# Kernel optimization log

Hardware: AMD Instinct MI355X
Metric: run time of the kernel (lower is better)

Reference implementation:

```python
import jax, jax.numpy as jnp
import numpy as np

H = 1024  # hidden_dims

def _gru_scan(xs, h0, wih, whh, bih, bhh):
    # xs: (T, D_in); torch GRU gate order: r, z, n
    xp = xs @ wih.T + bih  # (T, 3H), precomputed input projection
    def step(h, xp_t):
        hh = h @ whh.T + bhh
        r = jax.nn.sigmoid(xp_t[:H] + hh[:H])
        z = jax.nn.sigmoid(xp_t[H:2 * H] + hh[H:2 * H])
        n = jnp.tanh(xp_t[2 * H:] + r * hh[2 * H:])
        h_new = (1.0 - z) * n + z * h
        return h_new, None
    h_last, _ = jax.lax.scan(step, h0, xp)
    return h_last

def _lstm_step(h_in, wih, bih, bhh):
    # single-step nn.LSTM(H, H) with zero initial (h0, c0): Whh terms vanish, biases remain.
    # torch LSTM gate order: i, f, g, o
    xp = h_in @ wih.T + bih + bhh  # (4H,)
    i = jax.nn.sigmoid(xp[:H])
    g = jnp.tanh(xp[2 * H:3 * H])
    o = jax.nn.sigmoid(xp[3 * H:])
    c = i * g  # f * c0 == 0
    return o * jnp.tanh(c)

def setup_inputs() -> dict:
    key = jax.random.key(0)
    ks = jax.random.split(key, 20)
    T, D_w, D_i = 8192, 32, 32
    s = 0.05
    inp = {
        "weather_window": jax.random.normal(ks[0], (T, 1, D_w), jnp.float32),
        "infect_window": jax.random.normal(ks[1], (T, 1, D_i), jnp.float32),
        "time_window": jax.random.uniform(ks[2], (T, 1), jnp.float32),
        "h_init": jax.random.normal(ks[3], (1, 1, H), jnp.float32),
        "enc_w1": jax.random.normal(ks[4], (512, 64), jnp.float32) * s,
        "enc_b1": jax.random.normal(ks[5], (512,), jnp.float32) * s,
        "enc_w2": jax.random.normal(ks[6], (1024, 512), jnp.float32) * s,
        "enc_b2": jax.random.normal(ks[7], (1024,), jnp.float32) * s,
        "gru_wih": jax.random.normal(ks[8], (3 * H, H), jnp.float32) * s,
        "gru_whh": jax.random.normal(ks[9], (3 * H, H), jnp.float32) * s,
        "gru_bih": jax.random.normal(ks[10], (3 * H,), jnp.float32) * s,
        "gru_bhh": jax.random.normal(ks[11], (3 * H,), jnp.float32) * s,
        "lstm_wih": jax.random.normal(ks[12], (4 * H, H), jnp.float32) * s,
        "lstm_bih": jax.random.normal(ks[13], (4 * H,), jnp.float32) * s,
        "lstm_bhh": jax.random.normal(ks[14], (4 * H,), jnp.float32) * s,
        "dec_w1": jax.random.normal(ks[15], (512, 1024), jnp.float32) * s,
        "dec_b1": jax.random.normal(ks[16], (512,), jnp.float32) * s,
        "dec_w2": jax.random.normal(ks[17], (8, 512), jnp.float32) * s,
        "dec_b2": jax.random.normal(ks[18], (8,), jnp.float32) * s,
    }
    return inp

def reference(weather_window, infect_window, time_window, h_init,
              enc_w1, enc_b1, enc_w2, enc_b2,
              gru_wih, gru_whh, gru_bih, gru_bhh,
              lstm_wih, lstm_bih, lstm_bhh,
              dec_w1, dec_b1, dec_w2, dec_b2):
    T = weather_window.shape[0]
    # use_diff_time = False branch
    data_window = jnp.concatenate([weather_window, infect_window], axis=2)  # (T,1,64)
    rev = data_window[::-1]  # flip(0)
    # Encoder FC stack
    x = jax.nn.relu(rev @ enc_w1.T + enc_b1)
    x = jax.nn.relu(x @ enc_w2.T + enc_b2)  # (T,1,H)
    # Encoder GRU -> final hidden state
    h_enc = _gru_scan(x[:, 0, :], h_init[0, 0], gru_wih, gru_whh, gru_bih, gru_bhh)  # (H,)
    def step(h, _):
        h_new = _lstm_step(h, lstm_wih, lstm_bih, lstm_bhh)
        return h_new, h_new
    _, hs_tail = jax.lax.scan(step, h_enc, None, length=T - 1)  # (T-1, H)
    hs = jnp.concatenate([h_enc[None, :], hs_tail], axis=0)  # (T, H)
    hs = hs[:, None, None, :]  # (T,1,1,H), matches torch.stack of (1,1,H)
    # Decoder FC stack
    y = jax.nn.relu(hs @ dec_w1.T + dec_b1)
    y = y @ dec_w2.T + dec_b2  # (T,1,1,8)
    return y
```

## Files before the change

### kernel.cpp

```cpp
#include <hip/hip_runtime.h>
#include <hip/hip_bf16.h>
#include <math.h>

#define T_STEPS 8192
#define HDIM    1024
#define GW      128
#define NSLOT   512
#define SLOT_PITCH 256
#define NREP    8
#define REP_STRIDE ((size_t)2 * NSLOT * SLOT_PITCH)

#define OFF_REV   ((size_t)0)
#define OFF_X1    ((size_t)2097152)
#define OFF_B     ((size_t)18874368)
#define OFF_C     ((size_t)52428800)
#define WS_NEEDED ((size_t)153092096)

typedef float f4 __attribute__((ext_vector_type(4)));

__device__ inline float sigm(float x)   { return 1.0f / (1.0f + __expf(-x)); }
__device__ inline float tanh_f(float x) { float e = __expf(2.0f * x); return 1.0f - 2.0f / (e + 1.0f); }

__device__ inline f4* slot_ptr(char* base, int rep, int b, int k) {
    return (f4*)(base + (size_t)rep * REP_STRIDE + ((size_t)b * NSLOT + k) * SLOT_PITCH);
}

__device__ inline void store_cohr(f4* p, f4 v) {
    asm volatile("global_store_dwordx4 %0, %1, off sc0 sc1"
                 :: "v"(p), "v"(v) : "memory");
}

__device__ inline void poll_pair(const f4* p, unsigned want, f4& a, f4& b) {
    for (;;) {
        f4 va, vb;
        asm volatile("global_load_dwordx4 %0, %2, off sc0 sc1\n\t"
                     "global_load_dwordx4 %1, %2, off offset:256 sc0 sc1\n\t"
                     "s_waitcnt vmcnt(0)"
                     : "=&v"(va), "=&v"(vb) : "v"(p) : "memory");
        if (__float_as_uint(va.w) == want && __float_as_uint(vb.w) == want) {
            a = va; b = vb; return;
        }
        __builtin_amdgcn_s_sleep(1);
    }
}

__global__ void build_rev(const float* __restrict__ wea, const float* __restrict__ inf,
                          float* __restrict__ rev) {
    int idx = blockIdx.x * blockDim.x + threadIdx.x;
    if (idx >= T_STEPS * 64) return;
    int t = idx >> 6, c = idx & 63;
    int ts = T_STEPS - 1 - t;
    rev[idx] = (c < 32) ? wea[ts * 32 + c] : inf[ts * 32 + (c - 32)];
}

__global__ void seed_slots(const float* __restrict__ h0, char* __restrict__ sb) {
    int i = blockIdx.x * blockDim.x + threadIdx.x;
    int rep = i >> 10;
    int j   = i & 1023;
    if (rep < NREP) {
        if (j < NSLOT) {
            f4 v;
            v.x = h0[2 * j]; v.y = h0[2 * j + 1]; v.z = 0.0f;
            v.w = __uint_as_float(0u);
            store_cohr(slot_ptr(sb, rep, 0, j), v);
        } else {
            f4 v;
            v.x = 0.f; v.y = 0.f; v.z = 0.f;
            v.w = __uint_as_float(0xFFFFFFFFu);
            store_cohr(slot_ptr(sb, rep, 1, j - NSLOT), v);
        }
    }
}

__global__ __launch_bounds__(256) void gemm_bias_act(
    const float* __restrict__ A, const float* __restrict__ W,
    const float* __restrict__ bias, float* __restrict__ C,
    int M, int N, int K, int relu)
{
    __shared__ float As[32][68];
    __shared__ float Ws[32][68];
    const int tid = threadIdx.x;
    const int tx = tid & 15, ty = tid >> 4;
    const int bm = blockIdx.y, bn = blockIdx.x;
    const float* Ab = A + (size_t)bm * 64 * K;
    const float* Wb = W + (size_t)bn * 64 * K;
    float acc[4][4] = {};

    for (int k0 = 0; k0 < K; k0 += 32) {
#pragma unroll
        for (int q = 0; q < 2; ++q) {
            int idx = tid * 2 + q;
            int row = idx >> 3;
            int kc  = (idx & 7) << 2;
            float4 av = *(const float4*)(Ab + (size_t)row * K + k0 + kc);
            As[kc + 0][row] = av.x; As[kc + 1][row] = av.y;
            As[kc + 2][row] = av.z; As[kc + 3][row] = av.w;
            float4 wv = *(const float4*)(Wb + (size_t)row * K + k0 + kc);
            Ws[kc + 0][row] = wv.x; Ws[kc + 1][row] = wv.y;
            Ws[kc + 2][row] = wv.z; Ws[kc + 3][row] = wv.w;
        }
        __syncthreads();
#pragma unroll
        for (int k = 0; k < 32; ++k) {
            float4 a = *(const float4*)&As[k][ty << 2];
            float4 b = *(const float4*)&Ws[k][tx << 2];
            acc[0][0] += a.x*b.x; acc[0][1] += a.x*b.y; acc[0][2] += a.x*b.z; acc[0][3] += a.x*b.w;
            acc[1][0] += a.y*b.x; acc[1][1] += a.y*b.y; acc[1][2] += a.y*b.z; acc[1][3] += a.y*b.w;
            acc[2][0] += a.z*b.x; acc[2][1] += a.z*b.y; acc[2][2] += a.z*b.z; acc[2][3] += a.z*b.w;
            acc[3][0] += a.w*b.x; acc[3][1] += a.w*b.y; acc[3][2] += a.w*b.z; acc[3][3] += a.w*b.w;
        }
        __syncthreads();
    }

    int m0 = bm * 64 + (ty << 2), n0 = bn * 64 + (tx << 2);
    float4 bv = *(const float4*)(bias + n0);
#pragma unroll
    for (int r = 0; r < 4; ++r) {
        float4 o;
        o.x = acc[r][0] + bv.x; o.y = acc[r][1] + bv.y;
        o.z = acc[r][2] + bv.z; o.w = acc[r][3] + bv.w;
        if (relu) {
            o.x = fmaxf(o.x, 0.f); o.y = fmaxf(o.y, 0.f);
            o.z = fmaxf(o.z, 0.f); o.w = fmaxf(o.w, 0.f);
        }
        *(float4*)(C + (size_t)(m0 + r) * N + n0) = o;
    }
}

__global__ __launch_bounds__(256, 1) void gru_scan(
    const float* __restrict__ whh,
    const float* __restrict__ bhh,
    const float* __restrict__ xp,
    char* __restrict__ sb,
    float* __restrict__ hs)
{
    __shared__ float h_sh[2][HDIM];
    const int g = blockIdx.x, tid = threadIdx.x;
    const int w = tid >> 6, l = tid & 63;
    const int wv = g * 4 + w;
    const int rep = g & (NREP - 1);
    const int iA = 2 * wv, iB = iA + 1;
    const int rows[6] = { iA, HDIM + iA, 2*HDIM + iA, iB, HDIM + iB, 2*HDIM + iB };

    f4 Wf[6][4];
#pragma unroll
    for (int r = 0; r < 6; ++r) {
        const float* wr = whh + (size_t)rows[r] * HDIM + 4 * l;
#pragma unroll
        for (int j = 0; j < 4; ++j) Wf[r][j] = *(const f4*)(wr + 256 * j);
    }
#pragma unroll
    for (int r = 0; r < 6; ++r)
#pragma unroll
        for (int j = 0; j < 4; ++j)
            asm volatile("" : "+v"(Wf[r][j]));

    float b0 = 0.f, b1 = 0.f, b2 = 0.f;
    float xv0 = 0.f, xv1 = 0.f, xv2 = 0.f;
    int xrow = (l == 0) ? iA : iB;
    if (l < 2) {
        b0 = bhh[xrow]; b1 = bhh[HDIM + xrow]; b2 = bhh[2*HDIM + xrow];
        xv0 = xp[xrow]; xv1 = xp[HDIM + xrow]; xv2 = xp[2*HDIM + xrow];
    }

    for (int t = 0; t < T_STEPS; ++t) {
        const int buf = t & 1;
        f4 sa, sb2;
        poll_pair(slot_ptr(sb, rep, buf, 2 * tid), (unsigned)t, sa, sb2);
        h_sh[buf][4*tid + 0] = sa.x;  h_sh[buf][4*tid + 1] = sa.y;
        h_sh[buf][4*tid + 2] = sb2.x; h_sh[buf][4*tid + 3] = sb2.y;
        __syncthreads();

        f4 h4[4];
#pragma unroll
        for (int j = 0; j < 4; ++j) h4[j] = *(const f4*)&h_sh[buf][256*j + 4*l];

        float red[6];
#pragma unroll
        for (int r = 0; r < 6; ++r) {
            f4 p = Wf[r][0]*h4[0] + Wf[r][1]*h4[1] + Wf[r][2]*h4[2] + Wf[r][3]*h4[3];
            float v = p.x + p.y + p.z + p.w;
#pragma unroll
            for (int off = 32; off > 0; off >>= 1) v += __shfl_xor(v, off, 64);
            red[r] = v;
        }

        float hn = 0.f;
        if (l < 2) {
            float rd0 = (l == 0) ? red[0] : red[3];
            float rd1 = (l == 0) ? red[1] : red[4];
            float rd2 = (l == 0) ? red[2] : red[5];
            float hh_r = rd0 + b0, hh_z = rd1 + b1, hh_n = rd2 + b2;
            float r_ = sigm(xv0 + hh_r);
            float z_ = sigm(xv1 + hh_z);
            float n_ = tanh_f(xv2 + r_ * hh_n);
            float hp = h_sh[buf][xrow];
            hn = (1.0f - z_) * n_ + z_ * hp;
        }
        float hAv = __shfl(hn, 0, 64);
        float hBv = __shfl(hn, 1, 64);
        if (l < NREP) {
            unsigned pub = (unsigned)(t + 1);
            f4 s; s.x = hAv; s.y = hBv; s.z = 0.0f; s.w = __uint_as_float(pub);
            store_cohr(slot_ptr(sb, l, (int)(pub & 1), wv), s);
        }
        if (l == 0 && t == T_STEPS - 1) { hs[iA] = hAv; hs[iB] = hBv; }
        if (l < 2 && t + 1 < T_STEPS) {
            const float* xq = xp + (size_t)(t + 1) * (3 * HDIM);
            xv0 = xq[xrow]; xv1 = xq[HDIM + xrow]; xv2 = xq[2*HDIM + xrow];
        }
    }
}

__global__ __launch_bounds__(256, 1) void lstm_scan(
    const float* __restrict__ wih,
    const float* __restrict__ bih,
    const float* __restrict__ bhh,
    char* __restrict__ sb,
    float* __restrict__ hs)
{
    __shared__ float h_sh[2][HDIM];
    const int g = blockIdx.x, tid = threadIdx.x;
    const int w = tid >> 6, l = tid & 63;
    const int wv = g * 4 + w;
    const int rep = g & (NREP - 1);
    const int iA = 2 * wv, iB = iA + 1;
    const int rows[6] = { iA, 2*HDIM + iA, 3*HDIM + iA, iB, 2*HDIM + iB, 3*HDIM + iB };

    f4 Wf[6][4];
#pragma unroll
    for (int r = 0; r < 6; ++r) {
        const float* wr = wih + (size_t)rows[r] * HDIM + 4 * l;
#pragma unroll
        for (int j = 0; j < 4; ++j) Wf[r][j] = *(const f4*)(wr + 256 * j);
    }
#pragma unroll
    for (int r = 0; r < 6; ++r)
#pragma unroll
        for (int j = 0; j < 4; ++j)
            asm volatile("" : "+v"(Wf[r][j]));

    float b0 = 0.f, b1 = 0.f, b2 = 0.f;
    int xrow = (l == 0) ? iA : iB;
    if (l < 2) {
        b0 = bih[xrow]          + bhh[xrow];
        b1 = bih[2*HDIM + xrow] + bhh[2*HDIM + xrow];
        b2 = bih[3*HDIM + xrow] + bhh[3*HDIM + xrow];
    }

    for (int s = 1; s < T_STEPS; ++s) {
        const unsigned want = (unsigned)(8191 + s);
        const unsigned pub  = (unsigned)(8192 + s);
        const int buf = (int)(want & 1);
        f4 sa, sb2;
        poll_pair(slot_ptr(sb, rep, buf, 2 * tid), want, sa, sb2);
        h_sh[buf][4*tid + 0] = sa.x;  h_sh[buf][4*tid + 1] = sa.y;
        h_sh[buf][4*tid + 2] = sb2.x; h_sh[buf][4*tid + 3] = sb2.y;
        __syncthreads();

        f4 h4[4];
#pragma unroll
        for (int j = 0; j < 4; ++j) h4[j] = *(const f4*)&h_sh[buf][256*j + 4*l];

        float red[6];
#pragma unroll
        for (int r = 0; r < 6; ++r) {
            f4 p = Wf[r][0]*h4[0] + Wf[r][1]*h4[1] + Wf[r][2]*h4[2] + Wf[r][3]*h4[3];
            float v = p.x + p.y + p.z + p.w;
#pragma unroll
            for (int off = 32; off > 0; off >>= 1) v += __shfl_xor(v, off, 64);
            red[r] = v;
        }

        float hn = 0.f;
        if (l < 2) {
            float rd0 = (l == 0) ? red[0] : red[3];
            float rd1 = (l == 0) ? red[1] : red[4];
            float rd2 = (l == 0) ? red[2] : red[5];
            float i_ = sigm(rd0 + b0);
            float g_ = tanh_f(rd1 + b1);
            float o_ = sigm(rd2 + b2);
            hn = o_ * tanh_f(i_ * g_);
        }
        float hAv = __shfl(hn, 0, 64);
        float hBv = __shfl(hn, 1, 64);
        if (l < NREP) {
            f4 sv; sv.x = hAv; sv.y = hBv; sv.z = 0.0f; sv.w = __uint_as_float(pub);
            store_cohr(slot_ptr(sb, l, (int)(pub & 1), wv), sv);
        }
        if (l == 0) {
            hs[(size_t)s * HDIM + iA] = hAv;
            hs[(size_t)s * HDIM + iB] = hBv;
        }
    }
}

__global__ __launch_bounds__(256) void dec2_kernel(
    const float* __restrict__ y1,
    const float* __restrict__ w2,
    const float* __restrict__ b2,
    float* __restrict__ out)
{
    const int w = threadIdx.x >> 6, l = threadIdx.x & 63;
    const int t = blockIdx.x * 4 + w;
    const float* yr = y1 + (size_t)t * 512;
    float yv[8];
#pragma unroll
    for (int j = 0; j < 8; ++j) yv[j] = yr[l + 64 * j];
    float o[8];
#pragma unroll
    for (int n = 0; n < 8; ++n) {
        const float* wr = w2 + n * 512;
        float s = 0.f;
#pragma unroll
        for (int j = 0; j < 8; ++j) s += yv[j] * wr[l + 64 * j];
#pragma unroll
        for (int off = 32; off > 0; off >>= 1) s += __shfl_xor(s, off, 64);
        o[n] = s;
    }
    if (l == 0) {
#pragma unroll
        for (int n = 0; n < 8; ++n) out[(size_t)t * 8 + n] = o[n] + b2[n];
    }
}

extern "C" void kernel_launch(void* const* d_in, const int* in_sizes, int n_in,
                              void* d_out, int out_size, void* d_ws, size_t ws_size,
                              hipStream_t stream)
{
    const float* wea      = (const float*)d_in[0];
    const float* inf      = (const float*)d_in[1];
    const float* h_init   = (const float*)d_in[3];
    const float* enc_w1   = (const float*)d_in[4];
    const float* enc_b1   = (const float*)d_in[5];
    const float* enc_w2   = (const float*)d_in[6];
    const float* enc_b2   = (const float*)d_in[7];
    const float* gru_wih  = (const float*)d_in[8];
    const float* gru_whh  = (const float*)d_in[9];
    const float* gru_bih  = (const float*)d_in[10];
    const float* gru_bhh  = (const float*)d_in[11];
    const float* lstm_wih = (const float*)d_in[12];
    const float* lstm_bih = (const float*)d_in[13];
    const float* lstm_bhh = (const float*)d_in[14];
    const float* dec_w1   = (const float*)d_in[15];
    const float* dec_b1   = (const float*)d_in[16];
    const float* dec_w2   = (const float*)d_in[17];
    const float* dec_b2   = (const float*)d_in[18];

    if (ws_size < WS_NEEDED) return;

    char* ws = (char*)d_ws;
    float* rev   = (float*)(ws + OFF_REV);
    float* x1    = (float*)(ws + OFF_X1);
    float* x2    = (float*)(ws + OFF_B);
    float* hs    = (float*)(ws + OFF_B);
    float* xp    = (float*)(ws + OFF_C);
    float* y1    = (float*)(ws + OFF_C);
    char*  sb    = ws + OFF_X1;

    build_rev<<<(T_STEPS * 64) / 256, 256, 0, stream>>>(wea, inf, rev);

    gemm_bias_act<<<dim3(8, 128), 256, 0, stream>>>(rev, enc_w1, enc_b1, x1,
                                                    T_STEPS, 512, 64, 1);
    gemm_bias_act<<<dim3(16, 128), 256, 0, stream>>>(x1, enc_w2, enc_b2, x2,
                                                     T_STEPS, 1024, 512, 1);
    gemm_bias_act<<<dim3(48, 128), 256, 0, stream>>>(x2, gru_wih, gru_bih, xp,
                                                     T_STEPS, 3 * HDIM, HDIM, 0);
    seed_slots<<<32, 256, 0, stream>>>(h_init, sb);
    gru_scan<<<GW, 256, 0, stream>>>(gru_whh, gru_bhh, xp, sb, hs);
    lstm_scan<<<GW, 256, 0, stream>>>(lstm_wih, lstm_bih, lstm_bhh, sb, hs);

    gemm_bias_act<<<dim3(8, 128), 256, 0, stream>>>(hs, dec_w1, dec_b1, y1,
                                                    T_STEPS, 512, HDIM, 1);
    dec2_kernel<<<T_STEPS / 4, 256, 0, stream>>>(y1, dec_w2, dec_b2, (float*)d_out);
}
```

Measured before the change: 39.29 ms.

## Fuse GRU input projection and first decoder layer into persistent scan kernels

The GRU scan now keeps W_ih rows in registers and computes each step's input projection on the fly from x2. This removes the separate 8192x3072 projection GEMM and its round trip through memory. The LSTM scan also holds one decoder row per wave and writes relu(W1·h+b1) straight to y1, running one extra iteration so the last hidden state is covered; this drops the hs buffer and the decoder GEMM. In exchange each step does extra work inside the latency-bound scan loop, and register use roughly doubles in the GRU kernel, which risks spills.

After: 38.00 ms, median of 2. -3.3%, faster.

```diff
diff --git a/kernel.cpp b/kernel.cpp
--- a/kernel.cpp
+++ b/kernel.cpp
@@ -130,9 +130,10 @@
 __global__ __launch_bounds__(256, 1) void gru_scan(
     const float* __restrict__ whh,
     const float* __restrict__ bhh,
-    const float* __restrict__ xp,
-    char* __restrict__ sb,
-    float* __restrict__ hs)
+    const float* __restrict__ wih,
+    const float* __restrict__ bih,
+    const float* __restrict__ x2,
+    char* __restrict__ sb)
 {
     __shared__ float h_sh[2][HDIM];
     const int g = blockIdx.x, tid = threadIdx.x;
@@ -142,25 +143,53 @@
     const int iA = 2 * wv, iB = iA + 1;
     const int rows[6] = { iA, HDIM + iA, 2*HDIM + iA, iB, HDIM + iB, 2*HDIM + iB };
 
-    f4 Wf[6][4];
+    f4 Wf[6][4], Wi[6][4];
 #pragma unroll
     for (int r = 0; r < 6; ++r) {
         const float* wr = whh + (size_t)rows[r] * HDIM + 4 * l;
-#pragma unroll
-        for (int j = 0; j < 4; ++j) Wf[r][j] = *(const f4*)(wr + 256 * j);
+        const float* wr2 = wih + (size_t)rows[r] * HDIM + 4 * l;
+#pragma unroll
+        for (int j = 0; j < 4; ++j) {
+            Wf[r][j] = *(const f4*)(wr + 256 * j);
+            Wi[r][j] = *(const f4*)(wr2 + 256 * j);
+        }
     }
 #pragma unroll
     for (int r = 0; r < 6; ++r)
 #pragma unroll
-        for (int j = 0; j < 4; ++j)
+        for (int j = 0; j < 4; ++j) {
             asm volatile("" : "+v"(Wf[r][j]));
+            asm volatile("" : "+v"(Wi[r][j]));
+        }
 
     float b0 = 0.f, b1 = 0.f, b2 = 0.f;
+    float bi0 = 0.f, bi1 = 0.f, bi2 = 0.f;
     float xv0 = 0.f, xv1 = 0.f, xv2 = 0.f;
     int xrow = (l == 0) ? iA : iB;
     if (l < 2) {
-        b0 = bhh[xrow]; b1 = bhh[HDIM + xrow]; b2 = bhh[2*HDIM + xrow];
-        xv0 = xp[xrow]; xv1 = xp[HDIM + xrow]; xv2 = xp[2*HDIM + xrow];
+        b0  = bhh[xrow]; b1  = bhh[HDIM + xrow]; b2  = bhh[2*HDIM + xrow];
+        bi0 = bih[xrow]; bi1 = bih[HDIM + xrow]; bi2 = bih[2*HDIM + xrow];
+    }
+
+    {
+        const float* xr = x2 + 4 * l;
+        f4 x4p[4];
+#pragma unroll
+        for (int j = 0; j < 4; ++j) x4p[j] = *(const f4*)(xr + 256 * j);
+        float xred[6];
+#pragma unroll
+        for (int r = 0; r < 6; ++r) {
+            f4 p = Wi[r][0]*x4p[0] + Wi[r][1]*x4p[1] + Wi[r][2]*x4p[2] + Wi[r][3]*x4p[3];
+            float v = p.x + p.y + p.z + p.w;
+#pragma unroll
+            for (int off = 32; off > 0; off >>= 1) v += __shfl_xor(v, off, 64);
+            xred[r] = v;
+        }
+        if (l < 2) {
+            xv0 = ((l == 0) ? xred[0] : xred[3]) + bi0;
+            xv1 = ((l == 0) ? xred[1] : xred[4]) + bi1;
+            xv2 = ((l == 0) ? xred[2] : xred[5]) + bi2;
+        }
     }
 
     for (int t = 0; t < T_STEPS; ++t) {
@@ -204,10 +233,25 @@
             f4 s; s.x = hAv; s.y = hBv; s.z = 0.0f; s.w = __uint_as_float(pub);
             store_cohr(slot_ptr(sb, l, (int)(pub & 1), wv), s);
         }
-        if (l == 0 && t == T_STEPS - 1) { hs[iA] = hAv; hs[iB] = hBv; }
-        if (l < 2 && t + 1 < T_STEPS) {
-            const float* xq = xp + (size_t)(t + 1) * (3 * HDIM);
-            xv0 = xq[xrow]; xv1 = xq[HDIM + xrow]; xv2 = xq[2*HDIM + xrow];
+        if (t + 1 < T_STEPS) {
+            const float* xr = x2 + (size_t)(t + 1) * HDIM + 4 * l;
+            f4 x4p[4];
+#pragma unroll
+            for (int j = 0; j < 4; ++j) x4p[j] = *(const f4*)(xr + 256 * j);
+            float xred[6];
+#pragma unroll
+            for (int r = 0; r < 6; ++r) {
+                f4 p = Wi[r][0]*x4p[0] + Wi[r][1]*x4p[1] + Wi[r][2]*x4p[2] + Wi[r][3]*x4p[3];
+                float v = p.x + p.y + p.z + p.w;
+#pragma unroll
+                for (int off = 32; off > 0; off >>= 1) v += __shfl_xor(v, off, 64);
+                xred[r] = v;
+            }
+            if (l < 2) {
+                xv0 = ((l == 0) ? xred[0] : xred[3]) + bi0;
+                xv1 = ((l == 0) ? xred[1] : xred[4]) + bi1;
+                xv2 = ((l == 0) ? xred[2] : xred[5]) + bi2;
+            }
         }
     }
 }
@@ -216,8 +260,10 @@
     const float* __restrict__ wih,
     const float* __restrict__ bih,
     const float* __restrict__ bhh,
+    const float* __restrict__ w1,
+    const float* __restrict__ b1,
     char* __restrict__ sb,
-    float* __restrict__ hs)
+    float* __restrict__ y1)
 {
     __shared__ float h_sh[2][HDIM];
     const int g = blockIdx.x, tid = threadIdx.x;
@@ -234,21 +280,32 @@
 #pragma unroll
         for (int j = 0; j < 4; ++j) Wf[r][j] = *(const f4*)(wr + 256 * j);
     }
+    f4 Wd[4];
+    {
+        const float* wr = w1 + (size_t)wv * HDIM + 4 * l;
+#pragma unroll
+        for (int j = 0; j < 4; ++j) Wd[j] = *(const f4*)(wr + 256 * j);
+    }
 #pragma unroll
     for (int r = 0; r < 6; ++r)
 #pragma unroll
         for (int j = 0; j < 4; ++j)
             asm volatile("" : "+v"(Wf[r][j]));
-
-    float b0 = 0.f, b1 = 0.f, b2 = 0.f;
+#pragma unroll
+    for (int j = 0; j < 4; ++j)
+        asm volatile("" : "+v"(Wd[j]));
+
+    const float db = b1[wv];
+
+    float b0 = 0.f, b1_ = 0.f, b2 = 0.f;
     int xrow = (l == 0) ? iA : iB;
     if (l < 2) {
-        b0 = bih[xrow]          + bhh[xrow];
-        b1 = bih[2*HDIM + xrow] + bhh[2*HDIM + xrow];
-        b2 = bih[3*HDIM + xrow] + bhh[3*HDIM + xrow];
-    }
-
-    for (int s = 1; s < T_STEPS; ++s) {
+        b0  = bih[xrow]          + bhh[xrow];
+        b1_ = bih[2*HDIM + xrow] + bhh[2*HDIM + xrow];
+        b2  = bih[3*HDIM + xrow] + bhh[3*HDIM + xrow];
+    }
+
+    for (int s = 1; s <= T_STEPS; ++s) {
         const unsigned want = (unsigned)(8191 + s);
         const unsigned pub  = (unsigned)(8192 + s);
         const int buf = (int)(want & 1);
@@ -262,35 +319,42 @@
 #pragma unroll
         for (int j = 0; j < 4; ++j) h4[j] = *(const f4*)&h_sh[buf][256*j + 4*l];
 
-        float red[6];
-#pragma unroll
-        for (int r = 0; r < 6; ++r) {
-            f4 p = Wf[r][0]*h4[0] + Wf[r][1]*h4[1] + Wf[r][2]*h4[2] + Wf[r][3]*h4[3];
+        if (s < T_STEPS) {
+            float red[6];
+#pragma unroll
+            for (int r = 0; r < 6; ++r) {
+                f4 p = Wf[r][0]*h4[0] + Wf[r][1]*h4[1] + Wf[r][2]*h4[2] + Wf[r][3]*h4[3];
+                float v = p.x + p.y + p.z + p.w;
+#pragma unroll
+                for (int off = 32; off > 0; off >>= 1) v += __shfl_xor(v, off, 64);
+                red[r] = v;
+            }
+
+            float hn = 0.f;
+            if (l < 2) {
+                float rd0 = (l == 0) ? red[0] : red[3];
+                float rd1 = (l == 0) ? red[1] : red[4];
+                float rd2 = (l == 0) ? red[2] : red[5];
+                float i_ = sigm(rd0 + b0);
+                float g_ = tanh_f(rd1 + b1_);
+                float o_ = sigm(rd2 + b2);
+                hn = o_ * tanh_f(i_ * g_);
+            }
+            float hAv = __shfl(hn, 0, 64);
+            float hBv = __shfl(hn, 1, 64);
+            if (l < NREP) {
+                f4 sv; sv.x = hAv; sv.y = hBv; sv.z = 0.0f; sv.w = __uint_as_float(pub);
+                store_cohr(slot_ptr(sb, l, (int)(pub & 1), wv), sv);
+            }
+        }
+
+        {
+            f4 p = Wd[0]*h4[0] + Wd[1]*h4[1] + Wd[2]*h4[2] + Wd[3]*h4[3];
             float v = p.x + p.y + p.z + p.w;
 #pragma unroll
             for (int off = 32; off > 0; off >>= 1) v += __shfl_xor(v, off, 64);
-            red[r] = v;
-        }
-
-        float hn = 0.f;
-        if (l < 2) {
-            float rd0 = (l == 0) ? red[0] : red[3];
-            float rd1 = (l == 0) ? red[1] : red[4];
-            float rd2 = (l == 0) ? red[2] : red[5];
-            float i_ = sigm(rd0 + b0);
-            float g_ = tanh_f(rd1 + b1);
-            float o_ = sigm(rd2 + b2);
-            hn = o_ * tanh_f(i_ * g_);
-        }
-        float hAv = __shfl(hn, 0, 64);
-        float hBv = __shfl(hn, 1, 64);
-        if (l < NREP) {
-            f4 sv; sv.x = hAv; sv.y = hBv; sv.z = 0.0f; sv.w = __uint_as_float(pub);
-            store_cohr(slot_ptr(sb, l, (int)(pub & 1), wv), sv);
-        }
-        if (l == 0) {
-            hs[(size_t)s * HDIM + iA] = hAv;
-            hs[(size_t)s * HDIM + iB] = hBv;
+            if (l == 0)
+                y1[(size_t)(s - 1) * 512 + wv] = fmaxf(v + db, 0.f);
         }
     }
 }
@@ -353,8 +417,6 @@
     float* rev   = (float*)(ws + OFF_REV);
     float* x1    = (float*)(ws + OFF_X1);
     float* x2    = (float*)(ws + OFF_B);
-    float* hs    = (float*)(ws + OFF_B);
-    float* xp    = (float*)(ws + OFF_C);
     float* y1    = (float*)(ws + OFF_C);
     char*  sb    = ws + OFF_X1;
 
@@ -364,13 +426,10 @@
                                                     T_STEPS, 512, 64, 1);
     gemm_bias_act<<<dim3(16, 128), 256, 0, stream>>>(x1, enc_w2, enc_b2, x2,
                                                      T_STEPS, 1024, 512, 1);
-    gemm_bias_act<<<dim3(48, 128), 256, 0, stream>>>(x2, gru_wih, gru_bih, xp,
-                                                     T_STEPS, 3 * HDIM, HDIM, 0);
     seed_slots<<<32, 256, 0, stream>>>(h_init, sb);
-    gru_scan<<<GW, 256, 0, stream>>>(gru_whh, gru_bhh, xp, sb, hs);
-    lstm_scan<<<GW, 256, 0, stream>>>(lstm_wih, lstm_bih, lstm_bhh, sb, hs);
-
-    gemm_bias_act<<<dim3(8, 128), 256, 0, stream>>>(hs, dec_w1, dec_b1, y1,
-                                                    T_STEPS, 512, HDIM, 1);
+    gru_scan<<<GW, 256, 0, stream>>>(gru_whh, gru_bhh, gru_wih, gru_bih, x2, sb);
+    lstm_scan<<<GW, 256, 0, stream>>>(lstm_wih, lstm_bih, lstm_bhh,
+                                      dec_w1, dec_b1, sb, y1);
+
     dec2_kernel<<<T_STEPS / 4, 256, 0, stream>>>(y1, dec_w2, dec_b2, (float*)d_out);
 }
```
